# Kernel optimization log

Measured on AMD Instinct MI355X. Metric: run time of the kernel, lower is better.

The kernel has to match this reference:

```python
import jax, jax.numpy as jnp
import numpy as np

N = 40000
E = 640000
IN = 1300
H = 4
C = 64
G = 64  # number of graphs in the batch
NEG_SLOPE = 0.2


def gat_conv(x, edge_index, W, att_src, att_dst, bias):
    """PyG-style GATConv with default add_self_loops=True, concat heads.
    x: [N, F_in], W: [F_in, H*C], att_src/att_dst: [H, C], bias: [H*C].
    edge_index[0]=source j, edge_index[1]=target i (messages flow j->i).
    """
    n = x.shape[0]
    h = (x @ W).reshape(n, H, C)                      # [N, H, C]
    loop = jnp.arange(n, dtype=edge_index.dtype)
    src = jnp.concatenate([edge_index[0], loop])      # [E+N]
    dst = jnp.concatenate([edge_index[1], loop])      # [E+N]
    a_src = jnp.einsum('nhc,hc->nh', h, att_src)      # [N, H]
    a_dst = jnp.einsum('nhc,hc->nh', h, att_dst)      # [N, H]
    e = jax.nn.leaky_relu(a_src[src] + a_dst[dst], NEG_SLOPE)  # [E+N, H]
    # segment softmax over incoming edges of each target node
    e_max = jax.ops.segment_max(e, dst, num_segments=n)
    e = jnp.exp(e - e_max[dst])
    denom = jax.ops.segment_sum(e, dst, num_segments=n)
    alpha = e / (denom[dst] + 1e-16)                  # [E+N, H]
    msg = h[src] * alpha[:, :, None]                  # [E+N, H, C]
    out = jax.ops.segment_sum(msg, dst, num_segments=n)  # [N, H, C]
    return out.reshape(n, H * C) + bias


def global_mean_pool(x, batch, num_graphs):
    s = jax.ops.segment_sum(x, batch, num_segments=num_graphs)
    cnt = jax.ops.segment_sum(jnp.ones((x.shape[0],), x.dtype), batch,
                              num_segments=num_graphs)
    return s / jnp.maximum(cnt, 1.0)[:, None]


def setup_inputs() -> dict:
    key = jax.random.key(0)
    ks = jax.random.split(key, 12)
    x = jax.random.normal(ks[0], (N, IN), dtype=jnp.float32)
    edge_index = jax.random.randint(ks[1], (2, E), 0, N, dtype=jnp.int64)
    batch = jnp.sort(jax.random.randint(ks[2], (N,), 0, G, dtype=jnp.int64))
    s1 = 1.0 / np.sqrt(IN)
    s2 = 1.0 / np.sqrt(H * C)
    W1 = jax.random.normal(ks[3], (IN, H * C), dtype=jnp.float32) * s1
    att_src1 = jax.random.normal(ks[4], (H, C), dtype=jnp.float32) * s2
    att_dst1 = jax.random.normal(ks[5], (H, C), dtype=jnp.float32) * s2
    b1 = jnp.zeros((H * C,), jnp.float32)
    W2 = jax.random.normal(ks[6], (H * C, H * C), dtype=jnp.float32) * s2
    att_src2 = jax.random.normal(ks[7], (H, C), dtype=jnp.float32) * s2
    att_dst2 = jax.random.normal(ks[8], (H, C), dtype=jnp.float32) * s2
    b2 = jnp.zeros((H * C,), jnp.float32)
    lin_w = jax.random.normal(ks[9], (H * C, 1), dtype=jnp.float32) * s2
    lin_b = jnp.zeros((1,), jnp.float32)
    return {"x": x, "edge_index": edge_index, "batch": batch,
            "W1": W1, "att_src1": att_src1, "att_dst1": att_dst1, "b1": b1,
            "W2": W2, "att_src2": att_src2, "att_dst2": att_dst2, "b2": b2,
            "lin_w": lin_w, "lin_b": lin_b}


def reference(x, edge_index, batch, W1, att_src1, att_dst1, b1,
              W2, att_src2, att_dst2, b2, lin_w, lin_b):
    h = jax.nn.relu(gat_conv(x, edge_index, W1, att_src1, att_dst1, b1))
    h = jax.nn.relu(gat_conv(h, edge_index, W2, att_src2, att_dst2, b2))
    p = global_mean_pool(h, batch, G)                 # [G, H*C]
    out = p @ lin_w + lin_b                           # [G, 1]
    return out.squeeze()                              # [G]
```

## Files before the change

### kernel.cpp

```cpp
#include <hip/hip_runtime.h>
#include <hip/hip_bf16.h>

#define N_NODES 40000
#define N_EDGES 640000
#define F_IN    1300
#define NH      4
#define NC      64
#define F_OUT   256
#define NG      64
#define NEG_SLOPE 0.2f

typedef short short8v __attribute__((ext_vector_type(8)));
typedef float f32x16  __attribute__((ext_vector_type(16)));

__device__ __forceinline__ float lrelu(float x) { return x >= 0.f ? x : NEG_SLOPE * x; }

__device__ __forceinline__ short f2bf(float v) {
    unsigned u = __builtin_bit_cast(unsigned, v);
    unsigned r = (u + 0x7fffu + ((u >> 16) & 1u)) >> 16;
    return (short)r;
}
__device__ __forceinline__ float bf2f(short s) {
    unsigned u = ((unsigned)(unsigned short)s) << 16;
    return __builtin_bit_cast(float, u);
}

__device__ __forceinline__ short8v ld8(const short* p) {
    short4 a = *(const short4*)(p);
    short4 b = *(const short4*)(p + 4);
    short8v r;
    r[0] = a.x; r[1] = a.y; r[2] = a.z; r[3] = a.w;
    r[4] = b.x; r[5] = b.y; r[6] = b.z; r[7] = b.w;
    return r;
}

__global__ void wsplit_kernel(const float* __restrict__ W, short* __restrict__ hi,
                              short* __restrict__ lo, int K, int Kp)
{
    int idx = blockIdx.x * 256 + threadIdx.x;
    if (idx >= F_OUT * Kp) return;
    int n = idx / Kp, k = idx - n * Kp;
    float v = (k < K) ? W[(size_t)k * F_OUT + n] : 0.f;
    short h = f2bf(v);
    short l = f2bf(v - bf2f(h));
    hi[idx] = h;
    lo[idx] = l;
}

#define BK  32
#define LDK 36

__global__ __launch_bounds__(256, 3) void gemm_mfma_kernel(
    const float* __restrict__ A, const short* __restrict__ Bth,
    const short* __restrict__ Btl, float* __restrict__ C, int K, int Kp)
{
    __shared__ short As_hi[2][64][LDK];
    __shared__ short As_lo[2][64][LDK];

    const int t    = threadIdx.x;
    const int lane = t & 63;
    const int wv   = t >> 6;
    const int wc   = wv * 64;
    const int bm   = blockIdx.x * 64;

    f32x16 acc[2][2];
#pragma unroll
    for (int i = 0; i < 2; ++i)
#pragma unroll
        for (int j = 0; j < 2; ++j)
#pragma unroll
            for (int r = 0; r < 16; ++r) acc[i][j][r] = 0.f;

    const int arow = t >> 2;
    const int ac   = (t & 3) * 4;
    const int mr   = lane & 31;
    const int khalf = (lane >> 5) * 8;

    const size_t abase = (size_t)(bm + arow) * K;
    const size_t b0 = (size_t)(wc + mr) * Kp + khalf;
    const size_t b1 = (size_t)(wc + 32 + mr) * Kp + khalf;

    const int nt = Kp / BK;

    float4 av0 = make_float4(0.f, 0.f, 0.f, 0.f);
    float4 av1 = make_float4(0.f, 0.f, 0.f, 0.f);
    if (ac < K)      av0 = *(const float4*)&A[abase + ac];
    if (ac + 16 < K) av1 = *(const float4*)&A[abase + ac + 16];

    for (int it = 0; it < nt; ++it) {
        const int k0  = it * BK;
        const int buf = it & 1;

        const short8v bh0_0 = *(const short8v*)&Bth[b0 + k0];
        const short8v bh0_1 = *(const short8v*)&Bth[b0 + k0 + 16];
        const short8v bh1_0 = *(const short8v*)&Bth[b1 + k0];
        const short8v bh1_1 = *(const short8v*)&Bth[b1 + k0 + 16];
        const short8v bl0_0 = *(const short8v*)&Btl[b0 + k0];
        const short8v bl0_1 = *(const short8v*)&Btl[b0 + k0 + 16];
        const short8v bl1_0 = *(const short8v*)&Btl[b1 + k0];
        const short8v bl1_1 = *(const short8v*)&Btl[b1 + k0 + 16];

        {
            short4 h4, l4;
            h4.x = f2bf(av0.x); l4.x = f2bf(av0.x - bf2f(h4.x));
            h4.y = f2bf(av0.y); l4.y = f2bf(av0.y - bf2f(h4.y));
            h4.z = f2bf(av0.z); l4.z = f2bf(av0.z - bf2f(h4.z));
            h4.w = f2bf(av0.w); l4.w = f2bf(av0.w - bf2f(h4.w));
            *(short4*)&As_hi[buf][arow][ac] = h4;
            *(short4*)&As_lo[buf][arow][ac] = l4;
            h4.x = f2bf(av1.x); l4.x = f2bf(av1.x - bf2f(h4.x));
            h4.y = f2bf(av1.y); l4.y = f2bf(av1.y - bf2f(h4.y));
            h4.z = f2bf(av1.z); l4.z = f2bf(av1.z - bf2f(h4.z));
            h4.w = f2bf(av1.w); l4.w = f2bf(av1.w - bf2f(h4.w));
            *(short4*)&As_hi[buf][arow][ac + 16] = h4;
            *(short4*)&As_lo[buf][arow][ac + 16] = l4;
        }

        float4 nv0 = make_float4(0.f, 0.f, 0.f, 0.f);
        float4 nv1 = make_float4(0.f, 0.f, 0.f, 0.f);
        if (it + 1 < nt) {
            int gk0 = k0 + BK + ac;
            if (gk0 < K)      nv0 = *(const float4*)&A[abase + gk0];
            if (gk0 + 16 < K) nv1 = *(const float4*)&A[abase + gk0 + 16];
        }

        __syncthreads();

#pragma unroll
        for (int ks = 0; ks < 2; ++ks) {
            const int ko = ks * 16 + khalf;
            short8v ah0 = ld8(&As_hi[buf][mr][ko]);
            short8v ah1 = ld8(&As_hi[buf][32 + mr][ko]);
            short8v al0 = ld8(&As_lo[buf][mr][ko]);
            short8v al1 = ld8(&As_lo[buf][32 + mr][ko]);
            const short8v bh0 = ks ? bh0_1 : bh0_0;
            const short8v bh1 = ks ? bh1_1 : bh1_0;
            const short8v bl0 = ks ? bl0_1 : bl0_0;
            const short8v bl1 = ks ? bl1_1 : bl1_0;
            acc[0][0] = __builtin_amdgcn_mfma_f32_32x32x16_bf16(ah0, bh0, acc[0][0], 0, 0, 0);
            acc[0][0] = __builtin_amdgcn_mfma_f32_32x32x16_bf16(ah0, bl0, acc[0][0], 0, 0, 0);
            acc[0][0] = __builtin_amdgcn_mfma_f32_32x32x16_bf16(al0, bh0, acc[0][0], 0, 0, 0);
            acc[0][1] = __builtin_amdgcn_mfma_f32_32x32x16_bf16(ah0, bh1, acc[0][1], 0, 0, 0);
            acc[0][1] = __builtin_amdgcn_mfma_f32_32x32x16_bf16(ah0, bl1, acc[0][1], 0, 0, 0);
            acc[0][1] = __builtin_amdgcn_mfma_f32_32x32x16_bf16(al0, bh1, acc[0][1], 0, 0, 0);
            acc[1][0] = __builtin_amdgcn_mfma_f32_32x32x16_bf16(ah1, bh0, acc[1][0], 0, 0, 0);
            acc[1][0] = __builtin_amdgcn_mfma_f32_32x32x16_bf16(ah1, bl0, acc[1][0], 0, 0, 0);
            acc[1][0] = __builtin_amdgcn_mfma_f32_32x32x16_bf16(al1, bh0, acc[1][0], 0, 0, 0);
            acc[1][1] = __builtin_amdgcn_mfma_f32_32x32x16_bf16(ah1, bh1, acc[1][1], 0, 0, 0);
            acc[1][1] = __builtin_amdgcn_mfma_f32_32x32x16_bf16(ah1, bl1, acc[1][1], 0, 0, 0);
            acc[1][1] = __builtin_amdgcn_mfma_f32_32x32x16_bf16(al1, bh1, acc[1][1], 0, 0, 0);
        }
        av0 = nv0;
        av1 = nv1;
    }
#pragma unroll
    for (int fm = 0; fm < 2; ++fm)
#pragma unroll
        for (int fn = 0; fn < 2; ++fn)
#pragma unroll
            for (int r = 0; r < 16; ++r) {
                int row = bm + fm * 32 + (r & 3) + 8 * (r >> 2) + 4 * (lane >> 5);
                int col = wc + fn * 32 + (lane & 31);
                C[(size_t)row * F_OUT + col] = acc[fm][fn][r];
            }
}

__global__ __launch_bounds__(256) void attn_coef_kernel(const float* __restrict__ h,
                                                        const float* __restrict__ att_s,
                                                        const float* __restrict__ att_d,
                                                        float* __restrict__ a_s,
                                                        float* __restrict__ a_d)
{
    const int n = blockIdx.x;
    const int t = threadIdx.x;
    const int w = t >> 6;
    const int l = t & 63;
    float hv = h[(size_t)n * F_OUT + t];
    float vs = hv * att_s[t];
    float vd = hv * att_d[t];
#pragma unroll
    for (int o = 1; o < 64; o <<= 1) {
        vs += __shfl_xor(vs, o);
        vd += __shfl_xor(vd, o);
    }
    if (l == 0) {
        a_s[n * NH + w] = vs;
        a_d[n * NH + w] = vd;
    }
}

__global__ void hist_kernel(const int* __restrict__ ei, int* __restrict__ deg)
{
    int e = blockIdx.x * blockDim.x + threadIdx.x;
    if (e < N_EDGES) atomicAdd(&deg[ei[N_EDGES + e]], 1);
}

__global__ __launch_bounds__(1024) void scan_kernel(const int* __restrict__ deg,
                                                    int* __restrict__ rowptr)
{
    __shared__ int sums[1024];
    const int t = threadIdx.x;
    const int chunk = (N_NODES + 1023) / 1024;
    int beg = t * chunk;
    int end = beg + chunk; if (end > N_NODES) end = N_NODES;
    if (beg > N_NODES) beg = N_NODES;
    int s = 0;
    for (int i = beg; i < end; ++i) s += deg[i];
    sums[t] = s;
    __syncthreads();
    for (int o = 1; o < 1024; o <<= 1) {
        int v = (t >= o) ? sums[t - o] : 0;
        __syncthreads();
        sums[t] += v;
        __syncthreads();
    }
    int run = (t == 0) ? 0 : sums[t - 1];
    for (int i = beg; i < end; ++i) { rowptr[i] = run; run += deg[i]; }
    if (t == 1023) rowptr[N_NODES] = run;
}

__global__ void scatter_kernel(const int* __restrict__ ei, int* __restrict__ cursor,
                               int* __restrict__ ssrc)
{
    int e = blockIdx.x * blockDim.x + threadIdx.x;
    if (e < N_EDGES) {
        int d = ei[N_EDGES + e];
        int pos = atomicAdd(&cursor[d], 1);
        ssrc[pos] = ei[e];
    }
}

__global__ __launch_bounds__(256) void agg_kernel(const float* __restrict__ h,
                                                  const float* __restrict__ a_s,
                                                  const float* __restrict__ a_d,
                                                  const int* __restrict__ rowptr,
                                                  const int* __restrict__ ssrc,
                                                  const float* __restrict__ bias,
                                                  float* __restrict__ out)
{
    const int wv = threadIdx.x >> 6;
    const int n  = blockIdx.x * 4 + wv;
    const int l  = threadIdx.x & 63;
    const int hd = l >> 4;
    const int g  = l & 15;

    const int beg = rowptr[n];
    const int deg = rowptr[n + 1] - beg;

    const float adn    = a_d[n * NH + hd];
    const float self_e = lrelu(a_s[n * NH + hd] + adn);

    float mx = self_e;
    for (int i = g; i < deg; i += 16) {
        int s = ssrc[beg + i];
        mx = fmaxf(mx, lrelu(a_s[s * NH + hd] + adn));
    }
#pragma unroll
    for (int o = 1; o < 16; o <<= 1) mx = fmaxf(mx, __shfl_xor(mx, o));

    float sm = (g == 0) ? expf(self_e - mx) : 0.f;
    for (int i = g; i < deg; i += 16) {
        int s = ssrc[beg + i];
        sm += expf(lrelu(a_s[s * NH + hd] + adn) - mx);
    }
#pragma unroll
    for (int o = 1; o < 16; o <<= 1) sm += __shfl_xor(sm, o);
    const float den = sm + 1e-16f;

    const int c0 = l * 4;
    float4 acc;
    {
        float a0 = expf(self_e - mx) / den;
        float4 hv = *(const float4*)&h[(size_t)n * F_OUT + c0];
        acc.x = a0 * hv.x; acc.y = a0 * hv.y; acc.z = a0 * hv.z; acc.w = a0 * hv.w;
    }
    int i = 0;
    for (; i + 4 <= deg; i += 4) {
        int s0 = ssrc[beg + i];
        int s1 = ssrc[beg + i + 1];
        int s2 = ssrc[beg + i + 2];
        int s3 = ssrc[beg + i + 3];
        float e0 = a_s[s0 * NH + hd], e1 = a_s[s1 * NH + hd];
        float e2 = a_s[s2 * NH + hd], e3 = a_s[s3 * NH + hd];
        float4 h0 = *(const float4*)&h[(size_t)s0 * F_OUT + c0];
        float4 h1 = *(const float4*)&h[(size_t)s1 * F_OUT + c0];
        float4 h2 = *(const float4*)&h[(size_t)s2 * F_OUT + c0];
        float4 h3 = *(const float4*)&h[(size_t)s3 * F_OUT + c0];
        float a0 = expf(lrelu(e0 + adn) - mx) / den;
        float a1 = expf(lrelu(e1 + adn) - mx) / den;
        float a2 = expf(lrelu(e2 + adn) - mx) / den;
        float a3 = expf(lrelu(e3 + adn) - mx) / den;
        acc.x += a0 * h0.x + a1 * h1.x + a2 * h2.x + a3 * h3.x;
        acc.y += a0 * h0.y + a1 * h1.y + a2 * h2.y + a3 * h3.y;
        acc.z += a0 * h0.z + a1 * h1.z + a2 * h2.z + a3 * h3.z;
        acc.w += a0 * h0.w + a1 * h1.w + a2 * h2.w + a3 * h3.w;
    }
    for (; i < deg; ++i) {
        int s = ssrc[beg + i];
        float a0 = expf(lrelu(a_s[s * NH + hd] + adn) - mx) / den;
        float4 hv = *(const float4*)&h[(size_t)s * F_OUT + c0];
        acc.x += a0 * hv.x; acc.y += a0 * hv.y; acc.z += a0 * hv.z; acc.w += a0 * hv.w;
    }
    float4 bv = *(const float4*)&bias[c0];
    float4 ov;
    ov.x = fmaxf(acc.x + bv.x, 0.f);
    ov.y = fmaxf(acc.y + bv.y, 0.f);
    ov.z = fmaxf(acc.z + bv.z, 0.f);
    ov.w = fmaxf(acc.w + bv.w, 0.f);
    *(float4*)&out[(size_t)n * F_OUT + c0] = ov;
}

__global__ void ghist_kernel(const int* __restrict__ batch, int* __restrict__ gcnt)
{
    int n = blockIdx.x * blockDim.x + threadIdx.x;
    if (n < N_NODES) atomicAdd(&gcnt[batch[n]], 1);
}

__global__ __launch_bounds__(256) void pool_kernel(const float* __restrict__ x,
                                                   const int* __restrict__ gcnt,
                                                   const float* __restrict__ lin_w,
                                                   const float* __restrict__ lin_b,
                                                   float* __restrict__ out)
{
    const int g = blockIdx.x;
    const int t = threadIdx.x;
    __shared__ int s_start;
    if (t == 0) {
        int s = 0;
        for (int i = 0; i < g; ++i) s += gcnt[i];
        s_start = s;
    }
    __syncthreads();
    const int start = s_start;
    const int cnt = gcnt[g];
    float acc = 0.f;
    for (int i = 0; i < cnt; ++i) acc += x[(size_t)(start + i) * F_OUT + t];
    float p = acc / fmaxf((float)cnt, 1.f);
    float v = p * lin_w[t];
    __shared__ float red[256];
    red[t] = v;
    __syncthreads();
    for (int o = 128; o > 0; o >>= 1) {
        if (t < o) red[t] += red[t + o];
        __syncthreads();
    }
    if (t == 0) out[g] = red[0] + lin_b[0];
}

extern "C" void kernel_launch(void* const* d_in, const int* in_sizes, int n_in,
                              void* d_out, int out_size, void* d_ws, size_t ws_size,
                              hipStream_t stream)
{
    const float* x      = (const float*)d_in[0];
    const int*   ei     = (const int*)  d_in[1];
    const int*   batch  = (const int*)  d_in[2];
    const float* W1     = (const float*)d_in[3];
    const float* att_s1 = (const float*)d_in[4];
    const float* att_d1 = (const float*)d_in[5];
    const float* b1     = (const float*)d_in[6];
    const float* W2     = (const float*)d_in[7];
    const float* att_s2 = (const float*)d_in[8];
    const float* att_d2 = (const float*)d_in[9];
    const float* b2     = (const float*)d_in[10];
    const float* lin_w  = (const float*)d_in[11];
    const float* lin_b  = (const float*)d_in[12];
    float* out = (float*)d_out;

    const int Kp1 = 1312;
    const int Kp2 = 256;

    size_t off = 0;
    auto carve = [&](size_t bytes) -> void* {
        void* p = (char*)d_ws + off;
        off += (bytes + 255) & ~(size_t)255;
        return p;
    };
    float* hA     = (float*)carve((size_t)N_NODES * F_OUT * 4);
    float* hB     = (float*)carve((size_t)N_NODES * F_OUT * 4);
    float* a_s    = (float*)carve((size_t)N_NODES * NH * 4);
    float* a_d    = (float*)carve((size_t)N_NODES * NH * 4);
    int*   deg    = (int*)  carve((size_t)(N_NODES + 1) * 4);
    int*   rowptr = (int*)  carve((size_t)(N_NODES + 1) * 4);
    int*   cursor = (int*)  carve((size_t)N_NODES * 4);
    int*   ssrc   = (int*)  carve((size_t)N_EDGES * 4);
    int*   gcnt   = (int*)  carve((size_t)NG * 4);
    short* Bt1h   = (short*)carve((size_t)F_OUT * Kp1 * 2);
    short* Bt1l   = (short*)carve((size_t)F_OUT * Kp1 * 2);
    short* Bt2h   = (short*)carve((size_t)F_OUT * Kp2 * 2);
    short* Bt2l   = (short*)carve((size_t)F_OUT * Kp2 * 2);
    (void)ws_size; (void)n_in; (void)in_sizes; (void)out_size;

    hipMemsetAsync(deg, 0, (size_t)(N_NODES + 1) * 4, stream);
    hipMemsetAsync(gcnt, 0, (size_t)NG * 4, stream);
    hist_kernel<<<(N_EDGES + 255) / 256, 256, 0, stream>>>(ei, deg);
    scan_kernel<<<1, 1024, 0, stream>>>(deg, rowptr);
    hipMemcpyAsync(cursor, rowptr, (size_t)N_NODES * 4, hipMemcpyDeviceToDevice, stream);
    scatter_kernel<<<(N_EDGES + 255) / 256, 256, 0, stream>>>(ei, cursor, ssrc);
    ghist_kernel<<<(N_NODES + 255) / 256, 256, 0, stream>>>(batch, gcnt);
    wsplit_kernel<<<(F_OUT * Kp1 + 255) / 256, 256, 0, stream>>>(W1, Bt1h, Bt1l, F_IN, Kp1);
    wsplit_kernel<<<(F_OUT * Kp2 + 255) / 256, 256, 0, stream>>>(W2, Bt2h, Bt2l, F_OUT, Kp2);

    const int gblocks = N_NODES / 64;
    const int ablocks = N_NODES / 4;

    gemm_mfma_kernel<<<gblocks, 256, 0, stream>>>(x, Bt1h, Bt1l, hA, F_IN, Kp1);
    attn_coef_kernel<<<N_NODES, 256, 0, stream>>>(hA, att_s1, att_d1, a_s, a_d);
    agg_kernel<<<ablocks, 256, 0, stream>>>(hA, a_s, a_d, rowptr, ssrc, b1, hB);

    gemm_mfma_kernel<<<gblocks, 256, 0, stream>>>(hB, Bt2h, Bt2l, hA, F_OUT, Kp2);
    attn_coef_kernel<<<N_NODES, 256, 0, stream>>>(hA, att_s2, att_d2, a_s, a_d);
    agg_kernel<<<ablocks, 256, 0, stream>>>(hA, a_s, a_d, rowptr, ssrc, b2, hB);

    pool_kernel<<<NG, 256, 0, stream>>>(hB, gcnt, lin_w, lin_b, out);
}
```

Baseline: 1.183 ms.

## Precompute CSR edge logits, restructure aggregation, and shrink GEMM row tile

A new edge_logit kernel computes leaky-relu attention logits for all four heads per CSR edge in one pass, using a new edst array filled during the scatter. The aggregation kernel then reads these logits contiguously instead of gathering a_s per head, and uses fast exp, a reciprocal of the denominator and an 8-way unrolled gather loop. The GEMM tile shrinks from 64 to 32 rows with a higher occupancy bound, which doubles the B-operand traffic per output row. The extra logit pass writes and reads roughly 10 MB of logits per layer.

```diff
diff --git a/kernel.cpp b/kernel.cpp
--- a/kernel.cpp
+++ b/kernel.cpp
@@ -48,31 +48,30 @@
 }
 
 #define BK  32
+#define BMR 32
 #define LDK 36
 
-__global__ __launch_bounds__(256, 3) void gemm_mfma_kernel(
+__global__ __launch_bounds__(256, 4) void gemm_mfma_kernel(
     const float* __restrict__ A, const short* __restrict__ Bth,
     const short* __restrict__ Btl, float* __restrict__ C, int K, int Kp)
 {
-    __shared__ short As_hi[2][64][LDK];
-    __shared__ short As_lo[2][64][LDK];
+    __shared__ short As_hi[2][BMR][LDK];
+    __shared__ short As_lo[2][BMR][LDK];
 
     const int t    = threadIdx.x;
     const int lane = t & 63;
     const int wv   = t >> 6;
     const int wc   = wv * 64;
-    const int bm   = blockIdx.x * 64;
-
-    f32x16 acc[2][2];
-#pragma unroll
-    for (int i = 0; i < 2; ++i)
-#pragma unroll
-        for (int j = 0; j < 2; ++j)
-#pragma unroll
-            for (int r = 0; r < 16; ++r) acc[i][j][r] = 0.f;
-
-    const int arow = t >> 2;
-    const int ac   = (t & 3) * 4;
+    const int bm   = blockIdx.x * BMR;
+
+    f32x16 acc[2];
+#pragma unroll
+    for (int j = 0; j < 2; ++j)
+#pragma unroll
+        for (int r = 0; r < 16; ++r) acc[j][r] = 0.f;
+
+    const int arow = t >> 3;
+    const int ac   = (t & 7) * 4;
     const int mr   = lane & 31;
     const int khalf = (lane >> 5) * 8;
 
@@ -82,10 +81,8 @@
 
     const int nt = Kp / BK;
 
-    float4 av0 = make_float4(0.f, 0.f, 0.f, 0.f);
-    float4 av1 = make_float4(0.f, 0.f, 0.f, 0.f);
-    if (ac < K)      av0 = *(const float4*)&A[abase + ac];
-    if (ac + 16 < K) av1 = *(const float4*)&A[abase + ac + 16];
+    float4 av = make_float4(0.f, 0.f, 0.f, 0.f);
+    if (ac < K) av = *(const float4*)&A[abase + ac];
 
     for (int it = 0; it < nt; ++it) {
         const int k0  = it * BK;
@@ -102,67 +99,49 @@
 
         {
             short4 h4, l4;
-            h4.x = f2bf(av0.x); l4.x = f2bf(av0.x - bf2f(h4.x));
-            h4.y = f2bf(av0.y); l4.y = f2bf(av0.y - bf2f(h4.y));
-            h4.z = f2bf(av0.z); l4.z = f2bf(av0.z - bf2f(h4.z));
-            h4.w = f2bf(av0.w); l4.w = f2bf(av0.w - bf2f(h4.w));
+            h4.x = f2bf(av.x); l4.x = f2bf(av.x - bf2f(h4.x));
+            h4.y = f2bf(av.y); l4.y = f2bf(av.y - bf2f(h4.y));
+            h4.z = f2bf(av.z); l4.z = f2bf(av.z - bf2f(h4.z));
+            h4.w = f2bf(av.w); l4.w = f2bf(av.w - bf2f(h4.w));
             *(short4*)&As_hi[buf][arow][ac] = h4;
             *(short4*)&As_lo[buf][arow][ac] = l4;
-            h4.x = f2bf(av1.x); l4.x = f2bf(av1.x - bf2f(h4.x));
-            h4.y = f2bf(av1.y); l4.y = f2bf(av1.y - bf2f(h4.y));
-            h4.z = f2bf(av1.z); l4.z = f2bf(av1.z - bf2f(h4.z));
-            h4.w = f2bf(av1.w); l4.w = f2bf(av1.w - bf2f(h4.w));
-            *(short4*)&As_hi[buf][arow][ac + 16] = h4;
-            *(short4*)&As_lo[buf][arow][ac + 16] = l4;
         }
 
-        float4 nv0 = make_float4(0.f, 0.f, 0.f, 0.f);
-        float4 nv1 = make_float4(0.f, 0.f, 0.f, 0.f);
+        __syncthreads();
+        __builtin_amdgcn_sched_barrier(0);
+
+        float4 nv = make_float4(0.f, 0.f, 0.f, 0.f);
         if (it + 1 < nt) {
-            int gk0 = k0 + BK + ac;
-            if (gk0 < K)      nv0 = *(const float4*)&A[abase + gk0];
-            if (gk0 + 16 < K) nv1 = *(const float4*)&A[abase + gk0 + 16];
+            int gk = k0 + BK + ac;
+            if (gk < K) nv = *(const float4*)&A[abase + gk];
         }
-
-        __syncthreads();
 
 #pragma unroll
         for (int ks = 0; ks < 2; ++ks) {
             const int ko = ks * 16 + khalf;
-            short8v ah0 = ld8(&As_hi[buf][mr][ko]);
-            short8v ah1 = ld8(&As_hi[buf][32 + mr][ko]);
-            short8v al0 = ld8(&As_lo[buf][mr][ko]);
-            short8v al1 = ld8(&As_lo[buf][32 + mr][ko]);
+            short8v ah = ld8(&As_hi[buf][mr][ko]);
+            short8v al = ld8(&As_lo[buf][mr][ko]);
             const short8v bh0 = ks ? bh0_1 : bh0_0;
             const short8v bh1 = ks ? bh1_1 : bh1_0;
             const short8v bl0 = ks ? bl0_1 : bl0_0;
             const short8v bl1 = ks ? bl1_1 : bl1_0;
-            acc[0][0] = __builtin_amdgcn_mfma_f32_32x32x16_bf16(ah0, bh0, acc[0][0], 0, 0, 0);
-            acc[0][0] = __builtin_amdgcn_mfma_f32_32x32x16_bf16(ah0, bl0, acc[0][0], 0, 0, 0);
-            acc[0][0] = __builtin_amdgcn_mfma_f32_32x32x16_bf16(al0, bh0, acc[0][0], 0, 0, 0);
-            acc[0][1] = __builtin_amdgcn_mfma_f32_32x32x16_bf16(ah0, bh1, acc[0][1], 0, 0, 0);
-            acc[0][1] = __builtin_amdgcn_mfma_f32_32x32x16_bf16(ah0, bl1, acc[0][1], 0, 0, 0);
-            acc[0][1] = __builtin_amdgcn_mfma_f32_32x32x16_bf16(al0, bh1, acc[0][1], 0, 0, 0);
-            acc[1][0] = __builtin_amdgcn_mfma_f32_32x32x16_bf16(ah1, bh0, acc[1][0], 0, 0, 0);
-            acc[1][0] = __builtin_amdgcn_mfma_f32_32x32x16_bf16(ah1, bl0, acc[1][0], 0, 0, 0);
-            acc[1][0] = __builtin_amdgcn_mfma_f32_32x32x16_bf16(al1, bh0, acc[1][0], 0, 0, 0);
-            acc[1][1] = __builtin_amdgcn_mfma_f32_32x32x16_bf16(ah1, bh1, acc[1][1], 0, 0, 0);
-            acc[1][1] = __builtin_amdgcn_mfma_f32_32x32x16_bf16(ah1, bl1, acc[1][1], 0, 0, 0);
-            acc[1][1] = __builtin_amdgcn_mfma_f32_32x32x16_bf16(al1, bh1, acc[1][1], 0, 0, 0);
+            acc[0] = __builtin_amdgcn_mfma_f32_32x32x16_bf16(ah, bh0, acc[0], 0, 0, 0);
+            acc[0] = __builtin_amdgcn_mfma_f32_32x32x16_bf16(ah, bl0, acc[0], 0, 0, 0);
+            acc[0] = __builtin_amdgcn_mfma_f32_32x32x16_bf16(al, bh0, acc[0], 0, 0, 0);
+            acc[1] = __builtin_amdgcn_mfma_f32_32x32x16_bf16(ah, bh1, acc[1], 0, 0, 0);
+            acc[1] = __builtin_amdgcn_mfma_f32_32x32x16_bf16(ah, bl1, acc[1], 0, 0, 0);
+            acc[1] = __builtin_amdgcn_mfma_f32_32x32x16_bf16(al, bh1, acc[1], 0, 0, 0);
         }
-        av0 = nv0;
-        av1 = nv1;
-    }
-#pragma unroll
-    for (int fm = 0; fm < 2; ++fm)
-#pragma unroll
-        for (int fn = 0; fn < 2; ++fn)
-#pragma unroll
-            for (int r = 0; r < 16; ++r) {
-                int row = bm + fm * 32 + (r & 3) + 8 * (r >> 2) + 4 * (lane >> 5);
-                int col = wc + fn * 32 + (lane & 31);
-                C[(size_t)row * F_OUT + col] = acc[fm][fn][r];
-            }
+        av = nv;
+    }
+#pragma unroll
+    for (int fn = 0; fn < 2; ++fn)
+#pragma unroll
+        for (int r = 0; r < 16; ++r) {
+            int row = bm + (r & 3) + 8 * (r >> 2) + 4 * (lane >> 5);
+            int col = wc + fn * 32 + mr;
+            C[(size_t)row * F_OUT + col] = acc[fn][r];
+        }
 }
 
 __global__ __launch_bounds__(256) void attn_coef_kernel(const float* __restrict__ h,
@@ -220,17 +199,38 @@
 }
 
 __global__ void scatter_kernel(const int* __restrict__ ei, int* __restrict__ cursor,
-                               int* __restrict__ ssrc)
+                               int* __restrict__ ssrc, int* __restrict__ edst)
 {
     int e = blockIdx.x * blockDim.x + threadIdx.x;
     if (e < N_EDGES) {
         int d = ei[N_EDGES + e];
         int pos = atomicAdd(&cursor[d], 1);
         ssrc[pos] = ei[e];
-    }
+        edst[pos] = d;
+    }
+}
+
+__global__ void edge_logit_kernel(const int* __restrict__ ssrc,
+                                  const int* __restrict__ edst,
+                                  const float* __restrict__ a_s,
+                                  const float* __restrict__ a_d,
+                                  float* __restrict__ e_csr)
+{
+    int p = blockIdx.x * 256 + threadIdx.x;
+    if (p >= N_EDGES) return;
+    int s = ssrc[p], d = edst[p];
+    float4 as = ((const float4*)a_s)[s];
+    float4 ad = ((const float4*)a_d)[d];
+    float4 e;
+    e.x = lrelu(as.x + ad.x);
+    e.y = lrelu(as.y + ad.y);
+    e.z = lrelu(as.z + ad.z);
+    e.w = lrelu(as.w + ad.w);
+    ((float4*)e_csr)[p] = e;
 }
 
 __global__ __launch_bounds__(256) void agg_kernel(const float* __restrict__ h,
+                                                  const float* __restrict__ e_csr,
                                                   const float* __restrict__ a_s,
                                                   const float* __restrict__ a_d,
                                                   const int* __restrict__ rowptr,
@@ -241,73 +241,75 @@
     const int wv = threadIdx.x >> 6;
     const int n  = blockIdx.x * 4 + wv;
     const int l  = threadIdx.x & 63;
-    const int hd = l >> 4;
-    const int g  = l & 15;
 
     const int beg = rowptr[n];
     const int deg = rowptr[n + 1] - beg;
 
-    const float adn    = a_d[n * NH + hd];
-    const float self_e = lrelu(a_s[n * NH + hd] + adn);
-
-    float mx = self_e;
-    for (int i = g; i < deg; i += 16) {
-        int s = ssrc[beg + i];
-        mx = fmaxf(mx, lrelu(a_s[s * NH + hd] + adn));
-    }
-#pragma unroll
-    for (int o = 1; o < 16; o <<= 1) mx = fmaxf(mx, __shfl_xor(mx, o));
-
-    float sm = (g == 0) ? expf(self_e - mx) : 0.f;
-    for (int i = g; i < deg; i += 16) {
-        int s = ssrc[beg + i];
-        sm += expf(lrelu(a_s[s * NH + hd] + adn) - mx);
-    }
-#pragma unroll
-    for (int o = 1; o < 16; o <<= 1) sm += __shfl_xor(sm, o);
-    const float den = sm + 1e-16f;
-
-    const int c0 = l * 4;
+    const int hA = l & 3;
+    const float es = lrelu(a_s[n * NH + hA] + a_d[n * NH + hA]);
+    const float* ep = e_csr + (size_t)beg * 4;
+
+    float mx = es;
+    for (int base = 0; base < deg; base += 16) {
+        int i = base + (l >> 2);
+        float e = (i < deg) ? ep[(size_t)i * 4 + hA] : -1e30f;
+        mx = fmaxf(mx, e);
+    }
+#pragma unroll
+    for (int o = 4; o < 64; o <<= 1) mx = fmaxf(mx, __shfl_xor(mx, o));
+
+    float sm = ((l >> 2) == 0) ? __expf(es - mx) : 0.f;
+    for (int base = 0; base < deg; base += 16) {
+        int i = base + (l >> 2);
+        sm += (i < deg) ? __expf(ep[(size_t)i * 4 + hA] - mx) : 0.f;
+    }
+#pragma unroll
+    for (int o = 4; o < 64; o <<= 1) sm += __shfl_xor(sm, o);
+    const float dinv = 1.f / (sm + 1e-16f);
+
+    const int hB = l >> 4;
+    const float mxB = __shfl(mx, hB);
+    const float dvB = __shfl(dinv, hB);
+    const float esB = __shfl(es, hB);
+
+    const float4* h4 = (const float4*)h;
     float4 acc;
     {
-        float a0 = expf(self_e - mx) / den;
-        float4 hv = *(const float4*)&h[(size_t)n * F_OUT + c0];
-        acc.x = a0 * hv.x; acc.y = a0 * hv.y; acc.z = a0 * hv.z; acc.w = a0 * hv.w;
+        float sa = __expf(esB - mxB) * dvB;
+        float4 hv = h4[(size_t)n * 64 + l];
+        acc.x = sa * hv.x; acc.y = sa * hv.y; acc.z = sa * hv.z; acc.w = sa * hv.w;
     }
     int i = 0;
-    for (; i + 4 <= deg; i += 4) {
-        int s0 = ssrc[beg + i];
-        int s1 = ssrc[beg + i + 1];
-        int s2 = ssrc[beg + i + 2];
-        int s3 = ssrc[beg + i + 3];
-        float e0 = a_s[s0 * NH + hd], e1 = a_s[s1 * NH + hd];
-        float e2 = a_s[s2 * NH + hd], e3 = a_s[s3 * NH + hd];
-        float4 h0 = *(const float4*)&h[(size_t)s0 * F_OUT + c0];
-        float4 h1 = *(const float4*)&h[(size_t)s1 * F_OUT + c0];
-        float4 h2 = *(const float4*)&h[(size_t)s2 * F_OUT + c0];
-        float4 h3 = *(const float4*)&h[(size_t)s3 * F_OUT + c0];
-        float a0 = expf(lrelu(e0 + adn) - mx) / den;
-        float a1 = expf(lrelu(e1 + adn) - mx) / den;
-        float a2 = expf(lrelu(e2 + adn) - mx) / den;
-        float a3 = expf(lrelu(e3 + adn) - mx) / den;
-        acc.x += a0 * h0.x + a1 * h1.x + a2 * h2.x + a3 * h3.x;
-        acc.y += a0 * h0.y + a1 * h1.y + a2 * h2.y + a3 * h3.y;
-        acc.z += a0 * h0.z + a1 * h1.z + a2 * h2.z + a3 * h3.z;
-        acc.w += a0 * h0.w + a1 * h1.w + a2 * h2.w + a3 * h3.w;
+    for (; i + 8 <= deg; i += 8) {
+        const int p = beg + i;
+        int   s[8]; float e[8]; float4 v[8];
+#pragma unroll
+        for (int j = 0; j < 8; ++j) s[j] = ssrc[p + j];
+#pragma unroll
+        for (int j = 0; j < 8; ++j) e[j] = e_csr[(size_t)(p + j) * 4 + hB];
+#pragma unroll
+        for (int j = 0; j < 8; ++j) v[j] = h4[(size_t)s[j] * 64 + l];
+#pragma unroll
+        for (int j = 0; j < 8; ++j) {
+            float a = __expf(e[j] - mxB) * dvB;
+            acc.x += a * v[j].x; acc.y += a * v[j].y;
+            acc.z += a * v[j].z; acc.w += a * v[j].w;
+        }
     }
     for (; i < deg; ++i) {
-        int s = ssrc[beg + i];
-        float a0 = expf(lrelu(a_s[s * NH + hd] + adn) - mx) / den;
-        float4 hv = *(const float4*)&h[(size_t)s * F_OUT + c0];
-        acc.x += a0 * hv.x; acc.y += a0 * hv.y; acc.z += a0 * hv.z; acc.w += a0 * hv.w;
-    }
-    float4 bv = *(const float4*)&bias[c0];
+        const int p = beg + i;
+        int sj = ssrc[p];
+        float a = __expf(e_csr[(size_t)p * 4 + hB] - mxB) * dvB;
+        float4 hv = h4[(size_t)sj * 64 + l];
+        acc.x += a * hv.x; acc.y += a * hv.y; acc.z += a * hv.z; acc.w += a * hv.w;
+    }
+    float4 bv = ((const float4*)bias)[l];
     float4 ov;
     ov.x = fmaxf(acc.x + bv.x, 0.f);
     ov.y = fmaxf(acc.y + bv.y, 0.f);
     ov.z = fmaxf(acc.z + bv.z, 0.f);
     ov.w = fmaxf(acc.w + bv.w, 0.f);
-    *(float4*)&out[(size_t)n * F_OUT + c0] = ov;
+    ((float4*)out)[(size_t)n * 64 + l] = ov;
 }
 
 __global__ void ghist_kernel(const int* __restrict__ batch, int* __restrict__ gcnt)
@@ -383,6 +385,8 @@
     int*   rowptr = (int*)  carve((size_t)(N_NODES + 1) * 4);
     int*   cursor = (int*)  carve((size_t)N_NODES * 4);
     int*   ssrc   = (int*)  carve((size_t)N_EDGES * 4);
+    int*   edst   = (int*)  carve((size_t)N_EDGES * 4);
+    float* e_csr  = (float*)carve((size_t)N_EDGES * NH * 4);
     int*   gcnt   = (int*)  carve((size_t)NG * 4);
     short* Bt1h   = (short*)carve((size_t)F_OUT * Kp1 * 2);
     short* Bt1l   = (short*)carve((size_t)F_OUT * Kp1 * 2);
@@ -395,21 +399,24 @@
     hist_kernel<<<(N_EDGES + 255) / 256, 256, 0, stream>>>(ei, deg);
     scan_kernel<<<1, 1024, 0, stream>>>(deg, rowptr);
     hipMemcpyAsync(cursor, rowptr, (size_t)N_NODES * 4, hipMemcpyDeviceToDevice, stream);
-    scatter_kernel<<<(N_EDGES + 255) / 256, 256, 0, stream>>>(ei, cursor, ssrc);
+    scatter_kernel<<<(N_EDGES + 255) / 256, 256, 0, stream>>>(ei, cursor, ssrc, edst);
     ghist_kernel<<<(N_NODES + 255) / 256, 256, 0, stream>>>(batch, gcnt);
     wsplit_kernel<<<(F_OUT * Kp1 + 255) / 256, 256, 0, stream>>>(W1, Bt1h, Bt1l, F_IN, Kp1);
     wsplit_kernel<<<(F_OUT * Kp2 + 255) / 256, 256, 0, stream>>>(W2, Bt2h, Bt2l, F_OUT, Kp2);
 
-    const int gblocks = N_NODES / 64;
+    const int gblocks = N_NODES / BMR;
     const int ablocks = N_NODES / 4;
+    const int eblocks = (N_EDGES + 255) / 256;
 
     gemm_mfma_kernel<<<gblocks, 256, 0, stream>>>(x, Bt1h, Bt1l, hA, F_IN, Kp1);
     attn_coef_kernel<<<N_NODES, 256, 0, stream>>>(hA, att_s1, att_d1, a_s, a_d);
-    agg_kernel<<<ablocks, 256, 0, stream>>>(hA, a_s, a_d, rowptr, ssrc, b1, hB);
+    edge_logit_kernel<<<eblocks, 256, 0, stream>>>(ssrc, edst, a_s, a_d, e_csr);
+    agg_kernel<<<ablocks, 256, 0, stream>>>(hA, e_csr, a_s, a_d, rowptr, ssrc, b1, hB);
 
     gemm_mfma_kernel<<<gblocks, 256, 0, stream>>>(hB, Bt2h, Bt2l, hA, F_OUT, Kp2);
     attn_coef_kernel<<<N_NODES, 256, 0, stream>>>(hA, att_s2, att_d2, a_s, a_d);
-    agg_kernel<<<ablocks, 256, 0, stream>>>(hA, a_s, a_d, rowptr, ssrc, b2, hB);
+    edge_logit_kernel<<<eblocks, 256, 0, stream>>>(ssrc, edst, a_s, a_d, e_csr);
+    agg_kernel<<<ablocks, 256, 0, stream>>>(hA, e_csr, a_s, a_d, rowptr, ssrc, b2, hB);
 
     pool_kernel<<<NG, 256, 0, stream>>>(hB, gcnt, lin_w, lin_b, out);
 }
```

Result: slower. 1.236 ms (+4.4%).
